# Kernel optimization log

Hardware: AMD Instinct MI355X
Metric: run time of the kernel (lower is better)

## Reference

```python
import jax, jax.numpy as jnp
import numpy as np

N_LAYER = 4
N_HEAD = 16
N_EMBD = 1024
BLOCK = 1024
VOCAB = 100
TRANS = 16          # obs_dim + action_dim + 2 = 11 + 3 + 2
OBS_DIM = 11
ACT_DIM = 3
B, T = 2, 1024
VTOT = VOCAB * TRANS + 1  # token embedding rows
LN_EPS = 1e-5


def _layernorm(x, w, b):
    mu = jnp.mean(x, axis=-1, keepdims=True)
    var = jnp.var(x, axis=-1, keepdims=True)
    return (x - mu) * jax.lax.rsqrt(var + LN_EPS) * w + b


def _build_mask(t):
    # causal tril with every (joined_dim-1 mod joined_dim) column zeroed
    jd = OBS_DIM + ACT_DIM + 2  # 16
    m = jnp.tril(jnp.ones((t, t), dtype=bool))
    cols = jnp.arange(t)
    m = m & ((cols % jd) != (jd - 1))[None, :]
    return m  # [T, T] bool, True = keep


def setup_inputs() -> dict:
    key = jax.random.key(0)
    ks = jax.random.split(key, 24)
    C, L, F4 = N_EMBD, N_LAYER, 4 * N_EMBD
    g = lambda k, s: jax.random.normal(k, s, dtype=jnp.float32) * 0.02
    return {
        "tokens": jax.random.randint(ks[0], (B, T), 0, VTOT),
        "tok_emb": g(ks[1], (VTOT, C)),
        "pos_emb": g(ks[2], (1, BLOCK, C)),
        "Wq": g(ks[3], (L, C, C)), "bq": jnp.zeros((L, C), jnp.float32),
        "Wk": g(ks[4], (L, C, C)), "bk": jnp.zeros((L, C), jnp.float32),
        "Wv": g(ks[5], (L, C, C)), "bv": jnp.zeros((L, C), jnp.float32),
        "Wp": g(ks[6], (L, C, C)), "bp": jnp.zeros((L, C), jnp.float32),
        "ln1w": jnp.ones((L, C), jnp.float32), "ln1b": jnp.zeros((L, C), jnp.float32),
        "ln2w": jnp.ones((L, C), jnp.float32), "ln2b": jnp.zeros((L, C), jnp.float32),
        "W1": g(ks[7], (L, C, F4)), "b1": jnp.zeros((L, F4), jnp.float32),
        "W2": g(ks[8], (L, F4, C)), "b2": jnp.zeros((L, C), jnp.float32),
        "lnfw": jnp.ones((C,), jnp.float32), "lnfb": jnp.zeros((C,), jnp.float32),
        "head_w": g(ks[9], (TRANS, VOCAB + 1, C)),
    }


def _forward(tokens, tok_emb, pos_emb, Wq, bq, Wk, bk, Wv, bv, Wp, bp,
             ln1w, ln1b, ln2w, ln2b, W1, b1, W2, b2, lnfw, lnfb, head_w):
    b, t = tokens.shape
    C, H = N_EMBD, N_HEAD
    D = C // H
    scale = 1.0 / np.sqrt(D)
    mask = _build_mask(t)[None, None]  # [1,1,T,T]

    x = tok_emb[tokens] + pos_emb[:, :t, :]  # [B,T,C]
    for i in range(N_LAYER):
        h = _layernorm(x, ln1w[i], ln1b[i])
        q = (h @ Wq[i] + bq[i]).reshape(b, t, H, D).transpose(0, 2, 1, 3)
        k = (h @ Wk[i] + bk[i]).reshape(b, t, H, D).transpose(0, 2, 1, 3)
        v = (h @ Wv[i] + bv[i]).reshape(b, t, H, D).transpose(0, 2, 1, 3)
        att = jnp.einsum('bhtd,bhsd->bhts', q, k) * scale  # attn_bias=None => +0
        att = jnp.where(mask, att, -jnp.inf)
        att = jax.nn.softmax(att, axis=-1)
        y = jnp.einsum('bhts,bhsd->bhtd', att, v)
        y = y.transpose(0, 2, 1, 3).reshape(b, t, C)
        x = x + (y @ Wp[i] + bp[i])
        h2 = _layernorm(x, ln2w[i], ln2b[i])
        x = x + (jax.nn.gelu(h2 @ W1[i] + b1[i], approximate=False) @ W2[i] + b2[i])

    x = _layernorm(x, lnfw, lnfb)
    # pad_to_full_observation + EinLinear head
    n_pad = (TRANS - t % TRANS) % TRANS
    if n_pad:
        x = jnp.concatenate([x, jnp.zeros((b, n_pad, C), x.dtype)], axis=1)
    x_pad = x.reshape(-1, TRANS, C)                    # [b*n_states, TRANS, C]
    logits = jnp.einsum('eoi,bei->beo', head_w, x_pad)  # EinLinear, bias=False
    logits = logits.reshape(b, t + n_pad, VOCAB + 1)[:, :t]
    return logits


def reference(tokens, tok_emb, pos_emb, Wq, bq, Wk, bk, Wv, bv, Wp, bp,
              ln1w, ln1b, ln2w, ln2b, W1, b1, W2, b2, lnfw, lnfb, head_w):
    return _forward(tokens, tok_emb, pos_emb, Wq, bq, Wk, bk, Wv, bv, Wp, bp,
                    ln1w, ln1b, ln2w, ln2b, W1, b1, W2, b2, lnfw, lnfb, head_w)
```

## Files before the change

### kernel.cpp

```cpp
#include <hip/hip_runtime.h>
#include <hip/hip_bf16.h>
#include <math.h>

typedef unsigned short u16;
typedef __attribute__((ext_vector_type(8))) short short8;
typedef __attribute__((ext_vector_type(4))) short short4v;
typedef __attribute__((ext_vector_type(4))) float f32x4;

#define CDIM 1024
#define TDIM 1024
#define NROWS 2048
#define HEADS 16
#define HD 64
#define F4 4096

__device__ __forceinline__ u16 f2bf(float f) {
    union { float f; unsigned u; } v; v.f = f;
    unsigned r = v.u + 0x7fffu + ((v.u >> 16) & 1u);
    return (u16)(r >> 16);
}
__device__ __forceinline__ float bf2f(u16 h) {
    union { unsigned u; float f; } v; v.u = (unsigned)h << 16; return v.f;
}

__device__ __forceinline__ void gload_lds16(const void* g, void* lds) {
    __builtin_amdgcn_global_load_lds(
        (const __attribute__((address_space(1))) unsigned int*)g,
        (__attribute__((address_space(3))) unsigned int*)lds,
        16, 0, 0);
}

__device__ __forceinline__ void tile_map(int& bx, int& by, int& bz)
{
    const int gx = gridDim.x, gy = gridDim.y;
    const int fid = blockIdx.x + gx * (blockIdx.y + gy * blockIdx.z);
    const int nwg = gx * gy * gridDim.z;
    const int q = nwg >> 3, r = nwg & 7;
    const int xcd = fid & 7, t = fid >> 3;
    const int n = ((xcd < r) ? xcd * (q + 1) : r * (q + 1) + (xcd - r) * q) + t;
    const int nxy = gx * gy;
    bz = n / nxy;
    const int xy = n - bz * nxy;
    const int per_group = gx << 3;
    const int grp = xy / per_group;
    const int in = xy - grp * per_group;
    const int y0 = grp << 3;
    const int rem = gy - y0;
    const int gh = rem < 8 ? rem : 8;
    by = y0 + (in % gh);
    bx = in / gh;
}

__global__ __launch_bounds__(256)
void embed_k(const int* __restrict__ tok, const float* __restrict__ te,
             const float* __restrict__ pe, float* __restrict__ X)
{
    const int row = blockIdx.x;
    const int t = row & (TDIM - 1);
    const int tk = tok[row];
    const int c = threadIdx.x * 4;
    float4 a = *reinterpret_cast<const float4*>(te + (size_t)tk * CDIM + c);
    float4 b = *reinterpret_cast<const float4*>(pe + (size_t)t * CDIM + c);
    a.x += b.x; a.y += b.y; a.z += b.z; a.w += b.w;
    *reinterpret_cast<float4*>(X + (size_t)row * CDIM + c) = a;
}

template<bool BF16OUT>
__global__ __launch_bounds__(256)
void ln_k(const float* __restrict__ X, const float* __restrict__ g,
          const float* __restrict__ be, void* __restrict__ outp)
{
    __shared__ float red[4], red2[4];
    const int row = blockIdx.x, tid = threadIdx.x;
    const float* xr = X + (size_t)row * CDIM;
    const int c = tid * 4;
    float4 xv = *reinterpret_cast<const float4*>(xr + c);
    float s  = xv.x + xv.y + xv.z + xv.w;
    float s2 = xv.x*xv.x + xv.y*xv.y + xv.z*xv.z + xv.w*xv.w;
    #pragma unroll
    for (int off = 32; off; off >>= 1) {
        s  += __shfl_xor(s, off);
        s2 += __shfl_xor(s2, off);
    }
    if ((tid & 63) == 0) { red[tid >> 6] = s; red2[tid >> 6] = s2; }
    __syncthreads();
    const float ts  = red[0] + red[1] + red[2] + red[3];
    const float ts2 = red2[0] + red2[1] + red2[2] + red2[3];
    const float mu  = ts * (1.0f / CDIM);
    const float var = ts2 * (1.0f / CDIM) - mu * mu;
    const float rs  = rsqrtf(var + 1e-5f);
    float4 gv = *reinterpret_cast<const float4*>(g + c);
    float4 bv = *reinterpret_cast<const float4*>(be + c);
    float o0 = (xv.x - mu) * rs * gv.x + bv.x;
    float o1 = (xv.y - mu) * rs * gv.y + bv.y;
    float o2 = (xv.z - mu) * rs * gv.z + bv.z;
    float o3 = (xv.w - mu) * rs * gv.w + bv.w;
    if (BF16OUT) {
        u16 tmp[4] = { f2bf(o0), f2bf(o1), f2bf(o2), f2bf(o3) };
        u16* o = (u16*)outp + (size_t)row * CDIM + c;
        *reinterpret_cast<uint2*>(o) = *reinterpret_cast<const uint2*>(tmp);
    } else {
        float4 ov = { o0, o1, o2, o3 };
        *reinterpret_cast<float4*>((float*)outp + (size_t)row * CDIM + c) = ov;
    }
}

template<int MODE, int NZ>
__global__ __launch_bounds__(256)
void ln_red_k(float* __restrict__ X, const float* __restrict__ P,
              const float* __restrict__ g, const float* __restrict__ be,
              void* __restrict__ outp)
{
    __shared__ float red[4], red2[4];
    const int row = blockIdx.x, tid = threadIdx.x;
    const int c = tid * 4;
    float4 xv = *reinterpret_cast<const float4*>(X + (size_t)row * CDIM + c);
    #pragma unroll
    for (int z = 0; z < NZ; ++z) {
        float4 pv = *reinterpret_cast<const float4*>(P + ((size_t)z * NROWS + row) * CDIM + c);
        xv.x += pv.x; xv.y += pv.y; xv.z += pv.z; xv.w += pv.w;
    }
    if (MODE != 2)
        *reinterpret_cast<float4*>(X + (size_t)row * CDIM + c) = xv;
    float s  = xv.x + xv.y + xv.z + xv.w;
    float s2 = xv.x*xv.x + xv.y*xv.y + xv.z*xv.z + xv.w*xv.w;
    #pragma unroll
    for (int off = 32; off; off >>= 1) {
        s  += __shfl_xor(s, off);
        s2 += __shfl_xor(s2, off);
    }
    if ((tid & 63) == 0) { red[tid >> 6] = s; red2[tid >> 6] = s2; }
    __syncthreads();
    const float ts  = red[0] + red[1] + red[2] + red[3];
    const float ts2 = red2[0] + red2[1] + red2[2] + red2[3];
    const float mu  = ts * (1.0f / CDIM);
    const float var = ts2 * (1.0f / CDIM) - mu * mu;
    const float rs  = rsqrtf(var + 1e-5f);
    float4 gv = *reinterpret_cast<const float4*>(g + c);
    float4 bv = *reinterpret_cast<const float4*>(be + c);
    float o0 = (xv.x - mu) * rs * gv.x + bv.x;
    float o1 = (xv.y - mu) * rs * gv.y + bv.y;
    float o2 = (xv.z - mu) * rs * gv.z + bv.z;
    float o3 = (xv.w - mu) * rs * gv.w + bv.w;
    if (MODE == 0) {
        u16 tmp[4] = { f2bf(o0), f2bf(o1), f2bf(o2), f2bf(o3) };
        u16* o = (u16*)outp + (size_t)row * CDIM + c;
        *reinterpret_cast<uint2*>(o) = *reinterpret_cast<const uint2*>(tmp);
    } else {
        u16 hi[4] = { f2bf(o0), f2bf(o1), f2bf(o2), f2bf(o3) };
        u16 lo[4] = { f2bf(o0 - bf2f(hi[0])), f2bf(o1 - bf2f(hi[1])),
                      f2bf(o2 - bf2f(hi[2])), f2bf(o3 - bf2f(hi[3])) };
        const int b = row >> 10, p = row & 1023;
        const int e = p & 15, slot = p >> 4;
        u16* ar = (u16*)outp + (size_t)(e * 128 + b * 64 + slot) * 3072;
        *reinterpret_cast<uint2*>(ar + c)        = *reinterpret_cast<const uint2*>(hi);
        *reinterpret_cast<uint2*>(ar + 1024 + c) = *reinterpret_cast<const uint2*>(lo);
        *reinterpret_cast<uint2*>(ar + 2048 + c) = *reinterpret_cast<const uint2*>(hi);
    }
}

__global__ __launch_bounds__(256)
void convT_k(const float* __restrict__ W, u16* __restrict__ Wt,
             const int K, const int N)
{
    __shared__ u16 s[64][72];
    const int k0 = blockIdx.y * 64, n0 = blockIdx.x * 64;
    const int tr = threadIdx.x >> 4, tc = (threadIdx.x & 15) * 4;
    #pragma unroll
    for (int i = 0; i < 4; ++i) {
        int r = tr + i * 16;
        float4 w = *reinterpret_cast<const float4*>(W + (size_t)(k0 + r) * N + n0 + tc);
        s[r][tc + 0] = f2bf(w.x); s[r][tc + 1] = f2bf(w.y);
        s[r][tc + 2] = f2bf(w.z); s[r][tc + 3] = f2bf(w.w);
    }
    __syncthreads();
    #pragma unroll
    for (int i = 0; i < 4; ++i) {
        int n = tr + i * 16;
        u16 tmp[4];
        #pragma unroll
        for (int e = 0; e < 4; ++e) tmp[e] = s[tc + e][n];
        *reinterpret_cast<uint2*>(Wt + (size_t)(n0 + n) * K + k0 + tc) =
            *reinterpret_cast<const uint2*>(tmp);
    }
}

__global__ __launch_bounds__(256)
void convT3_k(const float* __restrict__ W0, const float* __restrict__ W1p,
              const float* __restrict__ W2p, u16* __restrict__ Wt)
{
    __shared__ u16 s[64][72];
    const float* W = blockIdx.z == 0 ? W0 : blockIdx.z == 1 ? W1p : W2p;
    u16* dst = Wt + (size_t)blockIdx.z * CDIM * CDIM;
    const int k0 = blockIdx.y * 64, n0 = blockIdx.x * 64;
    const int tr = threadIdx.x >> 4, tc = (threadIdx.x & 15) * 4;
    #pragma unroll
    for (int i = 0; i < 4; ++i) {
        int r = tr + i * 16;
        float4 w = *reinterpret_cast<const float4*>(W + (size_t)(k0 + r) * CDIM + n0 + tc);
        s[r][tc + 0] = f2bf(w.x); s[r][tc + 1] = f2bf(w.y);
        s[r][tc + 2] = f2bf(w.z); s[r][tc + 3] = f2bf(w.w);
    }
    __syncthreads();
    #pragma unroll
    for (int i = 0; i < 4; ++i) {
        int n = tr + i * 16;
        u16 tmp[4];
        #pragma unroll
        for (int e = 0; e < 4; ++e) tmp[e] = s[tc + e][n];
        *reinterpret_cast<uint2*>(dst + (size_t)(n0 + n) * CDIM + k0 + tc) =
            *reinterpret_cast<const uint2*>(tmp);
    }
}

__global__ __launch_bounds__(256)
void conv_head_k(const float* __restrict__ HW, u16* __restrict__ Wt)
{
    const int o = blockIdx.x, e = blockIdx.y;
    const int c = threadIdx.x * 4;
    u16 hi[4] = {0, 0, 0, 0}, lo[4] = {0, 0, 0, 0};
    if (o < 101) {
        float4 w = *reinterpret_cast<const float4*>(HW + ((size_t)e * 101 + o) * 1024 + c);
        hi[0] = f2bf(w.x); hi[1] = f2bf(w.y); hi[2] = f2bf(w.z); hi[3] = f2bf(w.w);
        lo[0] = f2bf(w.x - bf2f(hi[0])); lo[1] = f2bf(w.y - bf2f(hi[1]));
        lo[2] = f2bf(w.z - bf2f(hi[2])); lo[3] = f2bf(w.w - bf2f(hi[3]));
    }
    u16* wr = Wt + (size_t)(e * 128 + o) * 3072;
    *reinterpret_cast<uint2*>(wr + c)        = *reinterpret_cast<const uint2*>(hi);
    *reinterpret_cast<uint2*>(wr + 1024 + c) = *reinterpret_cast<const uint2*>(hi);
    *reinterpret_cast<uint2*>(wr + 2048 + c) = *reinterpret_cast<const uint2*>(lo);
}

__global__ __launch_bounds__(256)
void pack_bias_k(const float* __restrict__ a, const float* __restrict__ b,
                 const float* __restrict__ c, float* __restrict__ o)
{
    const int i = threadIdx.x * 4;
    const float* s = blockIdx.x == 0 ? a : blockIdx.x == 1 ? b : c;
    *reinterpret_cast<float4*>(o + (size_t)blockIdx.x * 1024 + i) =
        *reinterpret_cast<const float4*>(s + i);
}

template<int EPI>
__global__ __launch_bounds__(256, 2)
void gemm_bt(const u16* __restrict__ A, const u16* __restrict__ Bt,
             const float* __restrict__ bias, u16* __restrict__ outb,
             float* __restrict__ resid, u16* __restrict__ vtout,
             const int N, const int K, const int KCH)
{
    __shared__ __align__(16) u16 sA[2][2][128 * 32];
    __shared__ __align__(16) u16 sB[2][2][128 * 32];
    const int tid = threadIdx.x;
    const int lane = tid & 63, wv = tid >> 6;
    int bx, by, bz;
    tile_map(bx, by, bz);
    const int m0 = by * 128, n0 = bx * 128;
    const int kbeg = bz * KCH, kend = bz * KCH + KCH;
    const int fr = lane & 15, fq = lane >> 4;
    const int wm = wv & 1, wn = wv >> 1;
    const int srow = lane >> 2;
    const int schunk = (((lane & 3) ^ ((lane >> 3) & 3)) * 8);
    const int csw = (fr >> 1) & 3;
    const u16* Bt2 = (EPI == 3) ? Bt + (size_t)by * 128 * K : Bt;
    f32x4 acc[4][4] = {};

    float bias_r[4];
    #pragma unroll
    for (int nj = 0; nj < 4; ++nj) {
        const int col = n0 + wn * 64 + nj * 16 + fr;
        bias_r[nj] = (EPI == 3) ? 0.0f
                     : (EPI == 2 && bz != 0) ? 0.0f : bias[col];
    }

    auto stage = [&](int k0, int buf) {
        #pragma unroll
        for (int kk = 0; kk < 2; ++kk)
            #pragma unroll
            for (int i = 0; i < 2; ++i) {
                const int reg = i * 4 + wv;
                gload_lds16(A  + (size_t)(m0 + reg * 16 + srow) * K + k0 + kk * 32 + schunk,
                            &sA[buf][kk][reg * 512]);
                gload_lds16(Bt2 + (size_t)(n0 + reg * 16 + srow) * K + k0 + kk * 32 + schunk,
                            &sB[buf][kk][reg * 512]);
            }
    };

    asm volatile("s_waitcnt vmcnt(0)" ::: "memory");
    stage(kbeg, 0);
    int cur = 0;
    for (int k0 = kbeg; k0 < kend; k0 += 64) {
        asm volatile("s_waitcnt lgkmcnt(0)" ::: "memory");
        __builtin_amdgcn_s_barrier();
        if (k0 + 64 < kend) {
            stage(k0 + 64, cur ^ 1);
            asm volatile("s_waitcnt vmcnt(8)" ::: "memory");
        } else {
            asm volatile("s_waitcnt vmcnt(0)" ::: "memory");
        }
        __builtin_amdgcn_s_barrier();
        __builtin_amdgcn_s_setprio(1);
        #pragma unroll
        for (int kk = 0; kk < 2; ++kk) {
            short8 af[4], bf[4];
            #pragma unroll
            for (int mi = 0; mi < 4; ++mi)
                af[mi] = *reinterpret_cast<const short8*>(
                    &sA[cur][kk][(wm * 64 + mi * 16 + fr) * 32 + (fq ^ csw) * 8]);
            #pragma unroll
            for (int nj = 0; nj < 4; ++nj)
                bf[nj] = *reinterpret_cast<const short8*>(
                    &sB[cur][kk][(wn * 64 + nj * 16 + fr) * 32 + (fq ^ csw) * 8]);
            #pragma unroll
            for (int mi = 0; mi < 4; ++mi)
                #pragma unroll
                for (int nj = 0; nj < 4; ++nj)
                    acc[mi][nj] = __builtin_amdgcn_mfma_f32_16x16x32_bf16(af[mi], bf[nj], acc[mi][nj], 0, 0, 0);
        }
        __builtin_amdgcn_s_setprio(0);
        cur ^= 1;
    }

    #pragma unroll
    for (int nj = 0; nj < 4; ++nj) {
        const int col = n0 + wn * 64 + nj * 16 + fr;
        const float bias_v = bias_r[nj];
        #pragma unroll
        for (int mi = 0; mi < 4; ++mi) {
            const int rowb = m0 + wm * 64 + mi * 16 + fq * 4;
            if (EPI == 0 && vtout != nullptr && col >= 2048) {
                const int bidx = rowb >> 10, t = rowb & 1023, hd = col - 2048;
                u16 t4[4];
                #pragma unroll
                for (int r = 0; r < 4; ++r) t4[r] = f2bf(acc[mi][nj][r] + bias_v);
                *reinterpret_cast<uint2*>(
                    vtout + ((size_t)(bidx * 16 + (hd >> 6)) * 64 + (hd & 63)) * 1024 + t) =
                    *reinterpret_cast<const uint2*>(t4);
            } else {
                #pragma unroll
                for (int r = 0; r < 4; ++r) {
                    const int row = rowb + r;
                    float cv = acc[mi][nj][r] + bias_v;
                    if (EPI == 0) {
                        outb[(size_t)row * N + col] = f2bf(cv);
                    } else if (EPI == 1) {
                        float gl = 0.5f * cv * (1.0f + erff(cv * 0.70710678118654752f));
                        outb[(size_t)row * N + col] = f2bf(gl);
                    } else if (EPI == 2) {
                        resid[((size_t)bz * NROWS + row) * N + col] = cv;
                    } else {
                        resid[((size_t)bz * NROWS + row) * 128 + col] = cv;
                    }
                }
            }
        }
    }
}

__global__ __launch_bounds__(128)
void head_red_k(const float* __restrict__ P, float* __restrict__ out)
{
    const int pr = blockIdx.x;
    const int col = threadIdx.x;
    const int e = pr >> 7, rem = pr & 127, b = rem >> 6, slot = rem & 63;
    float s = 0.0f;
    #pragma unroll
    for (int z = 0; z < 8; ++z)
        s += P[((size_t)z * NROWS + pr) * 128 + col];
    if (col < 101)
        out[((size_t)(b << 10) + (slot << 4) + e) * 101 + col] = s;
}

__global__ __launch_bounds__(256, 4)
void attn_k(const u16* __restrict__ QKV, const u16* __restrict__ VT,
            float* __restrict__ po, float* __restrict__ plsum)
{
    __shared__ __align__(16) u16 sK[2][64][72];
    __shared__ __align__(16) u16 sV[2][64][72];
    const int tid = threadIdx.x, lane = tid & 63, wv = tid >> 6;
    const int fr = lane & 15, fq = lane >> 4;
    int bx, by, bz;
    tile_map(bx, by, bz);
    const int qt = bx, h = by, b = bz >> 2, sc = bz & 3;
    const int q0 = qt * 64;
    const int nt = qt + 1;
    const int stbeg = (nt * sc) >> 2, stend = (nt * (sc + 1)) >> 2;
    const u16* Qb = QKV + (size_t)b * TDIM * 3072 + h * HD;
    const u16* Vb = VT + ((size_t)(b * HEADS + h) * HD) * TDIM;
    const int r0 = tid >> 3, c0 = (tid & 7) * 8;

    const u16* qp = Qb + (size_t)(q0 + wv * 16 + fr) * 3072 + fq * 8;
    short8 aQ0 = *reinterpret_cast<const short8*>(qp);
    short8 aQ1 = *reinterpret_cast<const short8*>(qp + 32);

    f32x4 o[4] = {};
    float lsum = 0.0f;
    int cur = 0;

    if (stbeg < stend) {
        #pragma unroll
        for (int i = 0; i < 2; ++i) {
            const int r = r0 + i * 32;
            *reinterpret_cast<uint4*>(&sK[0][r][c0]) =
                *reinterpret_cast<const uint4*>(Qb + 1024 + (size_t)(stbeg * 64 + r) * 3072 + c0);
            *reinterpret_cast<uint4*>(&sV[0][r][c0]) =
                *reinterpret_cast<const uint4*>(Vb + (size_t)r * TDIM + stbeg * 64 + c0);
        }
        __syncthreads();
    }

    for (int st = stbeg; st < stend; ++st) {
        const int s0 = st * 64;
        const bool pf = (st + 1) < stend;
        uint4 pk[2], pv[2];
        if (pf) {
            #pragma unroll
            for (int i = 0; i < 2; ++i) {
                const int r = r0 + i * 32;
                pk[i] = *reinterpret_cast<const uint4*>(Qb + 1024 + (size_t)(s0 + 64 + r) * 3072 + c0);
                pv[i] = *reinterpret_cast<const uint4*>(Vb + (size_t)r * TDIM + s0 + 64 + c0);
            }
        }
        f32x4 sacc[4] = {};
        #pragma unroll
        for (int j = 0; j < 4; ++j) {
            short8 k0f = *reinterpret_cast<const short8*>(&sK[cur][j * 16 + fr][fq * 8]);
            sacc[j] = __builtin_amdgcn_mfma_f32_16x16x32_bf16(k0f, aQ0, sacc[j], 0, 0, 0);
            short8 k1f = *reinterpret_cast<const short8*>(&sK[cur][j * 16 + fr][32 + fq * 8]);
            sacc[j] = __builtin_amdgcn_mfma_f32_16x16x32_bf16(k1f, aQ1, sacc[j], 0, 0, 0);
        }
        const int qrow = q0 + wv * 16 + fr;
        u16 pb[4][4];
        #pragma unroll
        for (int j = 0; j < 4; ++j)
            #pragma unroll
            for (int r = 0; r < 4; ++r) {
                const int scol = s0 + j * 16 + fq * 4 + r;
                const bool keep = (scol <= qrow) && ((scol & 15) != 15);
                const float p = keep ? __expf(sacc[j][r] * 0.125f) : 0.0f;
                const u16 hb = f2bf(p);
                pb[j][r] = hb;
                lsum += bf2f(hb);
            }
        union { unsigned u[4]; short8 v; } a0, a1;
        a0.u[0] = (unsigned)pb[0][0] | ((unsigned)pb[0][1] << 16);
        a0.u[1] = (unsigned)pb[0][2] | ((unsigned)pb[0][3] << 16);
        a0.u[2] = (unsigned)pb[1][0] | ((unsigned)pb[1][1] << 16);
        a0.u[3] = (unsigned)pb[1][2] | ((unsigned)pb[1][3] << 16);
        a1.u[0] = (unsigned)pb[2][0] | ((unsigned)pb[2][1] << 16);
        a1.u[1] = (unsigned)pb[2][2] | ((unsigned)pb[2][3] << 16);
        a1.u[2] = (unsigned)pb[3][0] | ((unsigned)pb[3][1] << 16);
        a1.u[3] = (unsigned)pb[3][2] | ((unsigned)pb[3][3] << 16);
        #pragma unroll
        for (int j = 0; j < 4; ++j) {
            const u16* vrow = &sV[cur][j * 16 + fr][0];
            short4v v0 = *reinterpret_cast<const short4v*>(vrow + fq * 4);
            short4v v1 = *reinterpret_cast<const short4v*>(vrow + 16 + fq * 4);
            short8 bV0 = __builtin_shufflevector(v0, v1, 0, 1, 2, 3, 4, 5, 6, 7);
            o[j] = __builtin_amdgcn_mfma_f32_16x16x32_bf16(a0.v, bV0, o[j], 0, 0, 0);
            short4v v2 = *reinterpret_cast<const short4v*>(vrow + 32 + fq * 4);
            short4v v3 = *reinterpret_cast<const short4v*>(vrow + 48 + fq * 4);
            short8 bV1 = __builtin_shufflevector(v2, v3, 0, 1, 2, 3, 4, 5, 6, 7);
            o[j] = __builtin_amdgcn_mfma_f32_16x16x32_bf16(a1.v, bV1, o[j], 0, 0, 0);
        }
        if (pf) {
            #pragma unroll
            for (int i = 0; i < 2; ++i) {
                const int r = r0 + i * 32;
                *reinterpret_cast<uint4*>(&sK[cur ^ 1][r][c0]) = pk[i];
                *reinterpret_cast<uint4*>(&sV[cur ^ 1][r][c0]) = pv[i];
            }
            __syncthreads();
            cur ^= 1;
        }
    }

    lsum += __shfl_xor(lsum, 16);
    lsum += __shfl_xor(lsum, 32);

    const int tl = (bz * 16 + h) * 16 + qt;
    float* pt = po + (size_t)tl * 4096;
    #pragma unroll
    for (int j = 0; j < 4; ++j)
        #pragma unroll
        for (int r = 0; r < 4; ++r)
            pt[(wv * 16 + fq * 4 + r) * 64 + j * 16 + fr] = o[j][r];
    if (fq == 0) plsum[(size_t)tl * 64 + wv * 16 + fr] = lsum;
}

__global__ __launch_bounds__(256)
void attn_comb_k(const float* __restrict__ po, const float* __restrict__ plsum,
                 u16* __restrict__ Y)
{
    const int qt = blockIdx.x, h = blockIdx.y, b = blockIdx.z;
    int t[4];
    #pragma unroll
    for (int i = 0; i < 4; ++i) t[i] = ((b * 4 + i) * 16 + h) * 16 + qt;
    #pragma unroll
    for (int i = 0; i < 4; ++i) {
        const int f4 = threadIdx.x + i * 256;
        const int q = f4 >> 4, d4 = (f4 & 15) * 4;
        float4 a = *reinterpret_cast<const float4*>(po + (size_t)t[0] * 4096 + f4 * 4);
        float ls = plsum[(size_t)t[0] * 64 + q];
        #pragma unroll
        for (int k = 1; k < 4; ++k) {
            float4 c = *reinterpret_cast<const float4*>(po + (size_t)t[k] * 4096 + f4 * 4);
            a.x += c.x; a.y += c.y; a.z += c.z; a.w += c.w;
            ls += plsum[(size_t)t[k] * 64 + q];
        }
        const float rl = 1.0f / ls;
        u16 t4[4] = { f2bf(a.x * rl), f2bf(a.y * rl),
                      f2bf(a.z * rl), f2bf(a.w * rl) };
        *reinterpret_cast<uint2*>(
            Y + ((size_t)(b * TDIM + qt * 64 + q)) * CDIM + h * HD + d4) =
            *reinterpret_cast<const uint2*>(t4);
    }
}

extern "C" void kernel_launch(void* const* d_in, const int* in_sizes, int n_in,
                              void* d_out, int out_size, void* d_ws, size_t ws_size,
                              hipStream_t stream)
{
    const int*   tokens = (const int*)  d_in[0];
    const float* tok_emb= (const float*)d_in[1];
    const float* pos_emb= (const float*)d_in[2];
    const float* Wq = (const float*)d_in[3];
    const float* bq = (const float*)d_in[4];
    const float* Wk = (const float*)d_in[5];
    const float* bk = (const float*)d_in[6];
    const float* Wv = (const float*)d_in[7];
    const float* bv = (const float*)d_in[8];
    const float* Wp = (const float*)d_in[9];
    const float* bp = (const float*)d_in[10];
    const float* ln1w = (const float*)d_in[11];
    const float* ln1b = (const float*)d_in[12];
    const float* ln2w = (const float*)d_in[13];
    const float* ln2b = (const float*)d_in[14];
    const float* W1 = (const float*)d_in[15];
    const float* b1 = (const float*)d_in[16];
    const float* W2 = (const float*)d_in[17];
    const float* b2 = (const float*)d_in[18];
    const float* lnfw = (const float*)d_in[19];
    const float* lnfb = (const float*)d_in[20];
    const float* head_w = (const float*)d_in[21];
    float* out = (float*)d_out;

    char* ws = (char*)d_ws;
    float* x    = (float*)(ws);
    float* hpart= (float*)(ws);
    u16*   hbuf = (u16*)  (ws + (8u  << 20));
    u16*   yb   = (u16*)  (ws + (8u  << 20));
    u16*   qkv  = (u16*)  (ws + (12u << 20));
    u16*   xg   = (u16*)  (ws + (12u << 20));
    u16*   vt   = (u16*)  (ws + (24u << 20));
    u16*   mid  = (u16*)  (ws + (12u << 20));
    u16*   wbuf = (u16*)  (ws + (28u << 20));
    float* pbuf = (float*)(ws + (36u << 20));
    u16*   whp  = (u16*)  (ws + (36u << 20));
    float* po   = (float*)(ws + (36u << 20));
    float* plsum= (float*)(ws + (68u << 20));
    float* bbuf = (float*)(ws + (100u << 20));

    embed_k<<<NROWS, 256, 0, stream>>>(tokens, tok_emb, pos_emb, x);

    for (int l = 0; l < 4; ++l) {
        const size_t wo = (size_t)l * CDIM * CDIM;
        convT3_k<<<dim3(16, 16, 3), 256, 0, stream>>>(Wq + wo, Wk + wo, Wv + wo, wbuf);
        pack_bias_k<<<3, 256, 0, stream>>>(bq + l * CDIM, bk + l * CDIM, bv + l * CDIM, bbuf);

        if (l == 0)
            ln_k<true><<<NROWS, 256, 0, stream>>>(x, ln1w, ln1b, hbuf);
        else
            ln_red_k<0, 4><<<NROWS, 256, 0, stream>>>(x, pbuf, ln1w + l * CDIM, ln1b + l * CDIM, hbuf);
        gemm_bt<0><<<dim3(24, 16, 1), 256, 0, stream>>>(hbuf, wbuf, bbuf, qkv, nullptr, vt, 3072, CDIM, CDIM);
        attn_k<<<dim3(16, HEADS, 8), 256, 0, stream>>>(qkv, vt, po, plsum);
        attn_comb_k<<<dim3(16, HEADS, 2), 256, 0, stream>>>(po, plsum, yb);

        convT_k<<<dim3(16, 16), 256, 0, stream>>>(Wp + wo, wbuf, CDIM, CDIM);
        gemm_bt<2><<<dim3(8, 16, 2), 256, 0, stream>>>(yb, wbuf, bp + l * CDIM, nullptr, pbuf, nullptr, CDIM, CDIM, 512);

        ln_red_k<0, 2><<<NROWS, 256, 0, stream>>>(x, pbuf, ln2w + l * CDIM, ln2b + l * CDIM, hbuf);
        convT_k<<<dim3(64, 16), 256, 0, stream>>>(W1 + (size_t)l * CDIM * F4, wbuf, CDIM, F4);
        gemm_bt<1><<<dim3(32, 16, 1), 256, 0, stream>>>(hbuf, wbuf, b1 + l * F4, mid, nullptr, nullptr, F4, CDIM, CDIM);
        convT_k<<<dim3(16, 64), 256, 0, stream>>>(W2 + (size_t)l * F4 * CDIM, wbuf, F4, CDIM);
        gemm_bt<2><<<dim3(8, 16, 4), 256, 0, stream>>>(mid, wbuf, b2 + l * CDIM, nullptr, pbuf, nullptr, CDIM, F4, CDIM);
    }

    ln_red_k<2, 4><<<NROWS, 256, 0, stream>>>(x, pbuf, lnfw, lnfb, xg);
    conv_head_k<<<dim3(128, 16), 256, 0, stream>>>(head_w, whp);
    gemm_bt<3><<<dim3(1, 16, 8), 256, 0, stream>>>(xg, whp, nullptr, nullptr, hpart, nullptr, 128, 3072, 384);
    head_red_k<<<NROWS, 128, 0, stream>>>(hpart, out);
}
```

Baseline: 918.6 us.

## Hoist all weight conversions before the layer loop and widen head split-K

All per-layer weight transposes and bf16 conversions, plus the bias packing, now run once up front into separate per-layer workspace buffers. This replaces many small per-layer conversion launches with a few large ones that fill the device better. The workspace footprint grows substantially. The head GEMM split-K also doubles from 8 to 16 chunks, with the reduction kernel updated to match.

```diff
diff --git a/kernel.cpp b/kernel.cpp
--- a/kernel.cpp
+++ b/kernel.cpp
@@ -160,16 +160,19 @@
 }
 
 __global__ __launch_bounds__(256)
-void convT_k(const float* __restrict__ W, u16* __restrict__ Wt,
-             const int K, const int N)
+void convTL_k(const float* __restrict__ W, u16* __restrict__ Wt,
+              const int K, const int N)
 {
     __shared__ u16 s[64][72];
+    const int l = blockIdx.z;
+    const float* Wl = W + (size_t)l * K * N;
+    u16* dst = Wt + (size_t)l * K * N;
     const int k0 = blockIdx.y * 64, n0 = blockIdx.x * 64;
     const int tr = threadIdx.x >> 4, tc = (threadIdx.x & 15) * 4;
     #pragma unroll
     for (int i = 0; i < 4; ++i) {
         int r = tr + i * 16;
-        float4 w = *reinterpret_cast<const float4*>(W + (size_t)(k0 + r) * N + n0 + tc);
+        float4 w = *reinterpret_cast<const float4*>(Wl + (size_t)(k0 + r) * N + n0 + tc);
         s[r][tc + 0] = f2bf(w.x); s[r][tc + 1] = f2bf(w.y);
         s[r][tc + 2] = f2bf(w.z); s[r][tc + 3] = f2bf(w.w);
     }
@@ -180,26 +183,27 @@
         u16 tmp[4];
         #pragma unroll
         for (int e = 0; e < 4; ++e) tmp[e] = s[tc + e][n];
-        *reinterpret_cast<uint2*>(Wt + (size_t)(n0 + n) * K + k0 + tc) =
+        *reinterpret_cast<uint2*>(dst + (size_t)(n0 + n) * K + k0 + tc) =
             *reinterpret_cast<const uint2*>(tmp);
     }
 }
 
 __global__ __launch_bounds__(256)
-void convT3_k(const float* __restrict__ W0, const float* __restrict__ W1p,
-              const float* __restrict__ W2p, u16* __restrict__ Wt)
+void convT3L_k(const float* __restrict__ Wq, const float* __restrict__ Wk,
+               const float* __restrict__ Wv, u16* __restrict__ Wt)
 {
     __shared__ u16 s[64][72];
-    const float* W = blockIdx.z == 0 ? W0 : blockIdx.z == 1 ? W1p : W2p;
+    const int l = blockIdx.z / 3, w = blockIdx.z % 3;
+    const float* W = (w == 0 ? Wq : w == 1 ? Wk : Wv) + (size_t)l * CDIM * CDIM;
     u16* dst = Wt + (size_t)blockIdx.z * CDIM * CDIM;
     const int k0 = blockIdx.y * 64, n0 = blockIdx.x * 64;
     const int tr = threadIdx.x >> 4, tc = (threadIdx.x & 15) * 4;
     #pragma unroll
     for (int i = 0; i < 4; ++i) {
         int r = tr + i * 16;
-        float4 w = *reinterpret_cast<const float4*>(W + (size_t)(k0 + r) * CDIM + n0 + tc);
-        s[r][tc + 0] = f2bf(w.x); s[r][tc + 1] = f2bf(w.y);
-        s[r][tc + 2] = f2bf(w.z); s[r][tc + 3] = f2bf(w.w);
+        float4 wv4 = *reinterpret_cast<const float4*>(W + (size_t)(k0 + r) * CDIM + n0 + tc);
+        s[r][tc + 0] = f2bf(wv4.x); s[r][tc + 1] = f2bf(wv4.y);
+        s[r][tc + 2] = f2bf(wv4.z); s[r][tc + 3] = f2bf(wv4.w);
     }
     __syncthreads();
     #pragma unroll
@@ -232,11 +236,12 @@
 }
 
 __global__ __launch_bounds__(256)
-void pack_bias_k(const float* __restrict__ a, const float* __restrict__ b,
-                 const float* __restrict__ c, float* __restrict__ o)
-{
+void pack_bias_all_k(const float* __restrict__ a, const float* __restrict__ b,
+                     const float* __restrict__ c, float* __restrict__ o)
+{
+    const int l = blockIdx.x / 3, w = blockIdx.x % 3;
     const int i = threadIdx.x * 4;
-    const float* s = blockIdx.x == 0 ? a : blockIdx.x == 1 ? b : c;
+    const float* s = (w == 0 ? a : w == 1 ? b : c) + (size_t)l * 1024;
     *reinterpret_cast<float4*>(o + (size_t)blockIdx.x * 1024 + i) =
         *reinterpret_cast<const float4*>(s + i);
 }
@@ -364,7 +369,7 @@
     const int e = pr >> 7, rem = pr & 127, b = rem >> 6, slot = rem & 63;
     float s = 0.0f;
     #pragma unroll
-    for (int z = 0; z < 8; ++z)
+    for (int z = 0; z < 16; ++z)
         s += P[((size_t)z * NROWS + pr) * 128 + col];
     if (col < 101)
         out[((size_t)(b << 10) + (slot << 4) + e) * 101 + col] = s;
@@ -545,48 +550,54 @@
     float* out = (float*)d_out;
 
     char* ws = (char*)d_ws;
-    float* x    = (float*)(ws);
-    float* hpart= (float*)(ws);
-    u16*   hbuf = (u16*)  (ws + (8u  << 20));
-    u16*   yb   = (u16*)  (ws + (8u  << 20));
-    u16*   qkv  = (u16*)  (ws + (12u << 20));
-    u16*   xg   = (u16*)  (ws + (12u << 20));
-    u16*   vt   = (u16*)  (ws + (24u << 20));
-    u16*   mid  = (u16*)  (ws + (12u << 20));
-    u16*   wbuf = (u16*)  (ws + (28u << 20));
-    float* pbuf = (float*)(ws + (36u << 20));
-    u16*   whp  = (u16*)  (ws + (36u << 20));
-    float* po   = (float*)(ws + (36u << 20));
-    float* plsum= (float*)(ws + (68u << 20));
-    float* bbuf = (float*)(ws + (100u << 20));
+    float* x     = (float*)(ws);
+    float* hpart = (float*)(ws);
+    u16*   hbuf  = (u16*)  (ws + (8u   << 20));
+    u16*   yb    = (u16*)  (ws + (8u   << 20));
+    u16*   qkv   = (u16*)  (ws + (12u  << 20));
+    u16*   mid   = (u16*)  (ws + (12u  << 20));
+    u16*   xg    = (u16*)  (ws + (16u  << 20));
+    u16*   vt    = (u16*)  (ws + (24u  << 20));
+    u16*   wq_all= (u16*)  (ws + (28u  << 20));
+    u16*   wp_all= (u16*)  (ws + (52u  << 20));
+    u16*   w1_all= (u16*)  (ws + (60u  << 20));
+    u16*   w2_all= (u16*)  (ws + (92u  << 20));
+    u16*   whp   = (u16*)  (ws + (124u << 20));
+    float* pbuf  = (float*)(ws + (136u << 20));
+    float* po    = (float*)(ws + (136u << 20));
+    float* plsum = (float*)(ws + (168u << 20));
+    float* bbuf  = (float*)(ws + (169u << 20));
 
     embed_k<<<NROWS, 256, 0, stream>>>(tokens, tok_emb, pos_emb, x);
 
+    convT3L_k<<<dim3(16, 16, 12), 256, 0, stream>>>(Wq, Wk, Wv, wq_all);
+    convTL_k<<<dim3(16, 16, 4), 256, 0, stream>>>(Wp, wp_all, CDIM, CDIM);
+    convTL_k<<<dim3(64, 16, 4), 256, 0, stream>>>(W1, w1_all, CDIM, F4);
+    convTL_k<<<dim3(16, 64, 4), 256, 0, stream>>>(W2, w2_all, F4, CDIM);
+    pack_bias_all_k<<<12, 256, 0, stream>>>(bq, bk, bv, bbuf);
+    conv_head_k<<<dim3(128, 16), 256, 0, stream>>>(head_w, whp);
+
     for (int l = 0; l < 4; ++l) {
-        const size_t wo = (size_t)l * CDIM * CDIM;
-        convT3_k<<<dim3(16, 16, 3), 256, 0, stream>>>(Wq + wo, Wk + wo, Wv + wo, wbuf);
-        pack_bias_k<<<3, 256, 0, stream>>>(bq + l * CDIM, bk + l * CDIM, bv + l * CDIM, bbuf);
-
         if (l == 0)
             ln_k<true><<<NROWS, 256, 0, stream>>>(x, ln1w, ln1b, hbuf);
         else
             ln_red_k<0, 4><<<NROWS, 256, 0, stream>>>(x, pbuf, ln1w + l * CDIM, ln1b + l * CDIM, hbuf);
-        gemm_bt<0><<<dim3(24, 16, 1), 256, 0, stream>>>(hbuf, wbuf, bbuf, qkv, nullptr, vt, 3072, CDIM, CDIM);
+        gemm_bt<0><<<dim3(24, 16, 1), 256, 0, stream>>>(hbuf, wq_all + (size_t)l * 3 * CDIM * CDIM,
+                                                        bbuf + (size_t)l * 3072, qkv, nullptr, vt, 3072, CDIM, CDIM);
         attn_k<<<dim3(16, HEADS, 8), 256, 0, stream>>>(qkv, vt, po, plsum);
         attn_comb_k<<<dim3(16, HEADS, 2), 256, 0, stream>>>(po, plsum, yb);
 
-        convT_k<<<dim3(16, 16), 256, 0, stream>>>(Wp + wo, wbuf, CDIM, CDIM);
-        gemm_bt<2><<<dim3(8, 16, 2), 256, 0, stream>>>(yb, wbuf, bp + l * CDIM, nullptr, pbuf, nullptr, CDIM, CDIM, 512);
+        gemm_bt<2><<<dim3(8, 16, 2), 256, 0, stream>>>(yb, wp_all + (size_t)l * CDIM * CDIM,
+                                                       bp + l * CDIM, nullptr, pbuf, nullptr, CDIM, CDIM, 512);
 
         ln_red_k<0, 2><<<NROWS, 256, 0, stream>>>(x, pbuf, ln2w + l * CDIM, ln2b + l * CDIM, hbuf);
-        convT_k<<<dim3(64, 16), 256, 0, stream>>>(W1 + (size_t)l * CDIM * F4, wbuf, CDIM, F4);
-        gemm_bt<1><<<dim3(32, 16, 1), 256, 0, stream>>>(hbuf, wbuf, b1 + l * F4, mid, nullptr, nullptr, F4, CDIM, CDIM);
-        convT_k<<<dim3(16, 64), 256, 0, stream>>>(W2 + (size_t)l * F4 * CDIM, wbuf, F4, CDIM);
-        gemm_bt<2><<<dim3(8, 16, 4), 256, 0, stream>>>(mid, wbuf, b2 + l * CDIM, nullptr, pbuf, nullptr, CDIM, F4, CDIM);
+        gemm_bt<1><<<dim3(32, 16, 1), 256, 0, stream>>>(hbuf, w1_all + (size_t)l * CDIM * F4,
+                                                        b1 + l * F4, mid, nullptr, nullptr, F4, CDIM, CDIM);
+        gemm_bt<2><<<dim3(8, 16, 4), 256, 0, stream>>>(mid, w2_all + (size_t)l * CDIM * F4,
+                                                       b2 + l * CDIM, nullptr, pbuf, nullptr, CDIM, F4, CDIM);
     }
 
     ln_red_k<2, 4><<<NROWS, 256, 0, stream>>>(x, pbuf, lnfw, lnfb, xg);
-    conv_head_k<<<dim3(128, 16), 256, 0, stream>>>(head_w, whp);
-    gemm_bt<3><<<dim3(1, 16, 8), 256, 0, stream>>>(xg, whp, nullptr, nullptr, hpart, nullptr, 128, 3072, 384);
+    gemm_bt<3><<<dim3(1, 16, 16), 256, 0, stream>>>(xg, whp, nullptr, nullptr, hpart, nullptr, 128, 3072, 192);
     head_red_k<<<NROWS, 128, 0, stream>>>(hpart, out);
 }
```

After: 928.5 us. About the same (+1.1%).
